# Kernel tuning notes

Hardware: AMD Instinct MI355X
Metric: run time of the kernel (lower is better)

The kernel has to match this reference:

```python
import jax, jax.numpy as jnp
import numpy as np

# ---- config (mirrors cfg in __init__) ----
XB = (-51.2, 51.2, 0.2)
YB = (-51.2, 51.2, 0.2)
ZB = (-10.0, 10.0, 20.0)
C_BEV = 64
BN_EPS = 1e-5

DX = jnp.array([XB[2], YB[2], ZB[2]], jnp.float32)
BX = jnp.array([XB[0] + XB[2] / 2, YB[0] + YB[2] / 2, ZB[0] + ZB[2] / 2], jnp.float32)
NX = (int((XB[1] - XB[0]) / XB[2]), int((YB[1] - YB[0]) / YB[2]), int((ZB[1] - ZB[0]) / ZB[2]))  # (512, 512, 1)


def setup_inputs() -> dict:
    key = jax.random.key(0)
    k1, k2, k3, k4 = jax.random.split(key, 4)
    B, N = 4, 100000
    xy = jax.random.uniform(k1, (B, N, 2), jnp.float32, -54.0, 54.0)   # some points out of bounds
    z = jax.random.uniform(k2, (B, N, 1), jnp.float32, -3.0, 3.0)
    inten = jax.random.uniform(k3, (B, N, 1), jnp.float32)
    points = jnp.concatenate([xy, z, inten], axis=-1)
    W = jax.random.normal(k4, (4, C_BEV), jnp.float32) * 0.5
    b = jnp.zeros((C_BEV,), jnp.float32)
    gamma = jnp.ones((C_BEV,), jnp.float32)
    beta = jnp.zeros((C_BEV,), jnp.float32)
    return {"points": points, "W": W, "b": b, "gamma": gamma, "beta": beta}


def reference(points, W, b, gamma, beta):
    B, N, _ = points.shape
    nx, ny, nz = NX
    p = points.reshape(-1, 4)                      # (B*N, 4)

    # PFN: Linear + BatchNorm1d (training-mode batch stats, biased var) + ReLU
    h = p @ W + b                                  # (B*N, C)
    mu = jnp.mean(h, axis=0)
    var = jnp.var(h, axis=0)
    feat = jax.nn.relu(gamma * (h - mu) * jax.lax.rsqrt(var + BN_EPS) + beta)

    # grid coords: torch .long() truncates toward zero; jnp astype(int) does too
    coords = ((p[:, :3] - (BX - DX / 2.0)) / DX).astype(jnp.int32)
    kept = ((coords[:, 0] >= 0) & (coords[:, 0] < nx)
            & (coords[:, 1] >= 0) & (coords[:, 1] < ny)
            & (coords[:, 2] >= 0) & (coords[:, 2] < nz))

    batch_ix = jnp.repeat(jnp.arange(B, dtype=jnp.int32), N)
    ranks = (batch_ix * (nx * ny * nz)
             + coords[:, 0] + coords[:, 1] * nx + coords[:, 2] * (nx * ny))

    # invalid points -> sentinel bucket (jit-safe replacement for boolean filtering).
    # segment_sum per unique rank == the sort + QuickCumsum trick + scatter-assign.
    flat = B * nx * ny * nz
    ranks = jnp.where(kept, ranks, flat)
    feat = jnp.where(kept[:, None], feat, 0.0)
    bev = jax.ops.segment_sum(feat, ranks, num_segments=flat + 1)[:flat]  # (flat, C)

    bev = bev.reshape(B, nz, ny, nx, C_BEV)
    bev = jnp.transpose(bev, (0, 4, 1, 2, 3)).sum(axis=2)  # (B, C, ny, nx)
    return bev
```

## Files before the change

kernel.cpp:

```cpp
#include <hip/hip_runtime.h>


#define NXG 512
#define NYXG (512 * 512)
#define CB 64
#define SBLK 256

__device__ __forceinline__ int coord_mul5(float x, float offx) {
    float t = x - offx;
    asm volatile("" : "+v"(t));
    float q = t * 5.0f;
    asm volatile("" : "+v"(q));
    return (int)q;
}

__global__ void zero_ints(int* __restrict__ p, int n) {
    int i = blockIdx.x * blockDim.x + threadIdx.x;
    if (i < n) p[i] = 0;
}

__global__ void zero_kernel(float4* __restrict__ p, long n4) {
    long i = (long)blockIdx.x * blockDim.x + threadIdx.x;
    long stride = (long)gridDim.x * blockDim.x;
    float4 z = make_float4(0.f, 0.f, 0.f, 0.f);
    for (; i < n4; i += stride) p[i] = z;
}

__global__ void stats_count(const float4* __restrict__ pts, const float* __restrict__ W,
                            double* __restrict__ S_part, int* __restrict__ counts,
                            int M, int Nper) {
    __shared__ float4 tile[256];
    __shared__ double sh1[256], sh2[256];
    int t = threadIdx.x;
    int lane = t & 63;
    int wv = t >> 6;
    float w0 = W[lane], w1 = W[64 + lane], w2 = W[128 + lane], w3 = W[192 + lane];
    const float offx = -51.1f - 0.1f;
    double s1 = 0.0, s2 = 0.0;

    int chunk = (M + gridDim.x - 1) / gridDim.x;
    int base = blockIdx.x * chunk;
    int end = base + chunk; if (end > M) end = M;

    for (int i0 = base; i0 < end; i0 += 256) {
        int n = end - i0; if (n > 256) n = 256;
        __syncthreads();
        if (t < n) {
            float4 p = pts[i0 + t];
            tile[t] = p;
            int cx = coord_mul5(p.x, offx);
            int cy = coord_mul5(p.y, offx);
            if (cx >= 0 && cx < NXG && cy >= 0 && cy < NXG) {
                int b = (i0 + t) / Nper;
                int bin = (((b << 9) + cy) << 2) | (cx >> 7);
                atomicAdd(&counts[bin], 1);
            }
        }
        __syncthreads();
        int j0 = wv * 64, j1 = j0 + 64; if (j1 > n) j1 = n;
        for (int j = j0; j < j1; ++j) {
            float4 p = tile[j];
            float q = p.x * w0 + p.y * w1 + p.z * w2 + p.w * w3;
            double qd = (double)q;
            s1 += qd;
            s2 += qd * qd;
        }
    }
    sh1[t] = s1;
    sh2[t] = s2;
    __syncthreads();
    if (t < 64) {
        int c = t;
        S_part[(long)blockIdx.x * 128 + c] =
            (sh1[c] + sh1[64 + c]) + (sh1[128 + c] + sh1[192 + c]);
        S_part[(long)blockIdx.x * 128 + 64 + c] =
            (sh2[c] + sh2[64 + c]) + (sh2[128 + c] + sh2[192 + c]);
    }
}

__global__ void reduce_finalize(const double* __restrict__ S_part,
                                const float* __restrict__ gamma, const float* __restrict__ beta,
                                float* __restrict__ AB, double invM) {
    __shared__ double sh[4][128];
    __shared__ double tot[128];
    int t = threadIdx.x;
    int g = t >> 7, tt = t & 127;
    const double* base = S_part + (long)g * 64 * 128 + tt;
    double a0 = 0.0, a1 = 0.0, a2 = 0.0, a3 = 0.0;
#pragma unroll
    for (int b = 0; b < 64; b += 4) {
        a0 += base[(long)(b + 0) * 128];
        a1 += base[(long)(b + 1) * 128];
        a2 += base[(long)(b + 2) * 128];
        a3 += base[(long)(b + 3) * 128];
    }
    sh[g][tt] = (a0 + a1) + (a2 + a3);
    __syncthreads();
    if (t < 128) tot[t] = (sh[0][t] + sh[1][t]) + (sh[2][t] + sh[3][t]);
    __syncthreads();
    if (t < 64) {
        double mu = tot[t] * invM;
        double var = tot[64 + t] * invM - mu * mu;
        double sc = (double)gamma[t] / sqrt(var + 1e-5);
        AB[t] = (float)sc;
        AB[64 + t] = (float)((double)beta[t] - mu * sc);
    }
}

__global__ void scan_kernel(const int* __restrict__ counts, int* __restrict__ start,
                            int* __restrict__ cursor, int NB) {
    __shared__ int partial[256];
    int t = threadIdx.x;
    int chunk = (NB + 255) >> 8;
    int i0 = t * chunk;
    int i1 = i0 + chunk; if (i1 > NB) i1 = NB; if (i0 > NB) i0 = NB;
    int s = 0;
    for (int i = i0; i < i1; ++i) s += counts[i];
    partial[t] = s;
    __syncthreads();
    if (t == 0) {
        int run = 0;
        for (int k = 0; k < 256; ++k) { int v = partial[k]; partial[k] = run; run += v; }
    }
    __syncthreads();
    int run = partial[t];
    for (int i = i0; i < i1; ++i) {
        int v = counts[i];
        start[i] = run;
        cursor[i] = run;
        run += v;
    }
    if (t == 255) start[NB] = run;
}

__global__ void reorder_kernel(const float4* __restrict__ pts, int* __restrict__ cursor,
                               float4* __restrict__ pts_s, int M, int Nper) {
    int i = blockIdx.x * blockDim.x + threadIdx.x;
    int stride = gridDim.x * blockDim.x;
    const float offx = -51.1f - 0.1f;
    for (; i < M; i += stride) {
        float4 p = pts[i];
        int cx = coord_mul5(p.x, offx);
        int cy = coord_mul5(p.y, offx);
        if (cx < 0 || cx >= NXG || cy < 0 || cy >= NXG) continue;
        int b = i / Nper;
        int bin = (((b << 9) + cy) << 2) | (cx >> 7);
        int idx = atomicAdd(&cursor[bin], 1);
        pts_s[idx] = p;
    }
}

__global__ __launch_bounds__(256) void gather_out(
    const float4* __restrict__ pts_s, const float* __restrict__ W,
    const float* __restrict__ AB, const int* __restrict__ bin_start,
    float* __restrict__ out) {
    __shared__ float acc[CB][129];
    __shared__ float4 ptile[64];
    int t = threadIdx.x;
    int lane = t & 63, wv = t >> 6;
    int bin = blockIdx.x;
    int quarter = bin & 3;
    int y = (bin >> 2) & 511;
    int b = bin >> 11;

    for (int k = t; k < CB * 129; k += 256) ((float*)acc)[k] = 0.f;

    float w0 = W[lane], w1 = W[64 + lane], w2 = W[128 + lane], w3 = W[192 + lane];
    float A = AB[lane], Bc = AB[64 + lane];
    const float offx = -51.1f - 0.1f;
    int s = bin_start[bin], e = bin_start[bin + 1];

    for (int i0 = s; i0 < e; i0 += 64) {
        int nn = e - i0; if (nn > 64) nn = 64;
        __syncthreads();
        if (t < nn) ptile[t] = pts_s[i0 + t];
        __syncthreads();
        for (int j = wv; j < nn; j += 4) {
            float4 p = ptile[j];
            int cx = coord_mul5(p.x, offx);
            int x = cx - (quarter << 7);
            float q = p.x * w0 + p.y * w1 + p.z * w2 + p.w * w3;
            float f = fmaxf(q * A + Bc, 0.f);
            atomicAdd(&acc[lane][x], f);
        }
    }
    __syncthreads();

    size_t obase = (size_t)b * CB * NYXG + (size_t)y * NXG + (quarter << 7);
#pragma unroll
    for (int j = 0; j < 8; ++j) {
        int idx = j * 256 + t;
        int c = idx >> 5;
        int xq = (idx & 31) << 2;
        float4 v = make_float4(acc[c][xq], acc[c][xq + 1],
                               acc[c][xq + 2], acc[c][xq + 3]);
        *(float4*)(out + obase + (size_t)c * NYXG + xq) = v;
    }
}

__global__ void scatter_direct(const float4* __restrict__ pts, const float* __restrict__ W,
                               const float* __restrict__ AB, float* __restrict__ out,
                               int M, int Nper) {
    int lane = threadIdx.x & 63;
    int wid = blockIdx.x * (blockDim.x >> 6) + (threadIdx.x >> 6);
    int nw = gridDim.x * (blockDim.x >> 6);
    float w0 = W[lane], w1 = W[64 + lane], w2 = W[128 + lane], w3 = W[192 + lane];
    float A = AB[lane], Bc = AB[64 + lane];
    const float offx = -51.1f - 0.1f;
    for (int i = wid; i < M; i += nw) {
        float4 p = pts[i];
        int cx = coord_mul5(p.x, offx);
        int cy = coord_mul5(p.y, offx);
        if (cx < 0 || cx >= NXG || cy < 0 || cy >= NXG) continue;
        int b = i / Nper;
        float q = p.x * w0 + p.y * w1 + p.z * w2 + p.w * w3;
        float f = fmaxf(q * A + Bc, 0.f);
        atomicAdd(&out[((long)(b * CB + lane) * NXG + cy) * NXG + cx], f);
    }
}

extern "C" void kernel_launch(void* const* d_in, const int* in_sizes, int n_in,
                              void* d_out, int out_size, void* d_ws, size_t ws_size,
                              hipStream_t stream) {
    const float4* pts = (const float4*)d_in[0];
    const float* W = (const float*)d_in[1];
    const float* gamma = (const float*)d_in[3];
    const float* beta = (const float*)d_in[4];
    float* out = (float*)d_out;

    int M = in_sizes[0] / 4;
    int B = out_size / (CB * NYXG);
    int Nper = M / B;
    int NB = B * 2048;

    char* wsb = (char*)d_ws;
    float* AB = (float*)(wsb + 1024);
    double* S_part = (double*)(wsb + 2048);

    size_t off = 2048 + (size_t)SBLK * 128 * sizeof(double);
    int* counts = (int*)(wsb + off);     off += (size_t)NB * 4;
    int* bin_start = (int*)(wsb + off);  off += (size_t)(NB + 1) * 4;
    int* bin_cursor = (int*)(wsb + off); off += (size_t)NB * 4;
    off = (off + 15) & ~(size_t)15;
    float4* pts_s = (float4*)(wsb + off); off += (size_t)M * 16;
    size_t need = off;

    if (ws_size >= need) {
        zero_ints<<<(NB + 255) / 256, 256, 0, stream>>>(counts, NB);
        stats_count<<<SBLK, 256, 0, stream>>>(pts, W, S_part, counts, M, Nper);
        reduce_finalize<<<1, 512, 0, stream>>>(S_part, gamma, beta, AB, 1.0 / (double)M);
        scan_kernel<<<1, 256, 0, stream>>>(counts, bin_start, bin_cursor, NB);
        reorder_kernel<<<1024, 256, 0, stream>>>(pts, bin_cursor, pts_s, M, Nper);
        gather_out<<<NB, 256, 0, stream>>>(pts_s, W, AB, bin_start, out);
    } else {
        zero_kernel<<<2048, 256, 0, stream>>>((float4*)out, (long)out_size / 4);
        stats_count<<<SBLK, 256, 0, stream>>>(pts, W, S_part, (int*)(wsb + 2048), M, Nper);
        reduce_finalize<<<1, 512, 0, stream>>>(S_part, gamma, beta, AB, 1.0 / (double)M);
        scatter_direct<<<2048, 256, 0, stream>>>(pts, W, AB, out, M, Nper);
    }
}
```

Measured before the change: 250.9 us.

## Restructure gather so each block owns one channel over a 16-row BEV strip

Points are now binned per (batch, row) instead of per (batch, row, x-quarter). The gather kernel assigns one block per (batch, 16-row strip, channel) and keeps a 16x512 shared accumulator, so each thread processes points independently with conflict-light shared atomics and writes one contiguous 32KB output region. The cost is that every point in a strip is re-read and re-projected once per channel, 64 times in total, in exchange for fully coalesced channel-plane stores and no per-point tile sync.

```diff
diff --git a/kernel.cpp b/kernel.cpp
--- a/kernel.cpp
+++ b/kernel.cpp
@@ -5,6 +5,7 @@
 #define NYXG (512 * 512)
 #define CB 64
 #define SBLK 256
+#define YCH 16
 
 __device__ __forceinline__ int coord_mul5(float x, float offx) {
     float t = x - offx;
@@ -52,8 +53,7 @@
             int cy = coord_mul5(p.y, offx);
             if (cx >= 0 && cx < NXG && cy >= 0 && cy < NXG) {
                 int b = (i0 + t) / Nper;
-                int bin = (((b << 9) + cy) << 2) | (cx >> 7);
-                atomicAdd(&counts[bin], 1);
+                atomicAdd(&counts[(b << 9) | cy], 1);
             }
         }
         __syncthreads();
@@ -144,8 +144,7 @@
         int cy = coord_mul5(p.y, offx);
         if (cx < 0 || cx >= NXG || cy < 0 || cy >= NXG) continue;
         int b = i / Nper;
-        int bin = (((b << 9) + cy) << 2) | (cx >> 7);
-        int idx = atomicAdd(&cursor[bin], 1);
+        int idx = atomicAdd(&cursor[(b << 9) | cy], 1);
         pts_s[idx] = p;
     }
 }
@@ -154,48 +153,37 @@
     const float4* __restrict__ pts_s, const float* __restrict__ W,
     const float* __restrict__ AB, const int* __restrict__ bin_start,
     float* __restrict__ out) {
-    __shared__ float acc[CB][129];
-    __shared__ float4 ptile[64];
-    int t = threadIdx.x;
-    int lane = t & 63, wv = t >> 6;
-    int bin = blockIdx.x;
-    int quarter = bin & 3;
-    int y = (bin >> 2) & 511;
-    int b = bin >> 11;
-
-    for (int k = t; k < CB * 129; k += 256) ((float*)acc)[k] = 0.f;
-
-    float w0 = W[lane], w1 = W[64 + lane], w2 = W[128 + lane], w3 = W[192 + lane];
-    float A = AB[lane], Bc = AB[64 + lane];
-    const float offx = -51.1f - 0.1f;
-    int s = bin_start[bin], e = bin_start[bin + 1];
-
-    for (int i0 = s; i0 < e; i0 += 64) {
-        int nn = e - i0; if (nn > 64) nn = 64;
-        __syncthreads();
-        if (t < nn) ptile[t] = pts_s[i0 + t];
-        __syncthreads();
-        for (int j = wv; j < nn; j += 4) {
-            float4 p = ptile[j];
-            int cx = coord_mul5(p.x, offx);
-            int x = cx - (quarter << 7);
-            float q = p.x * w0 + p.y * w1 + p.z * w2 + p.w * w3;
-            float f = fmaxf(q * A + Bc, 0.f);
-            atomicAdd(&acc[lane][x], f);
-        }
-    }
-    __syncthreads();
-
-    size_t obase = (size_t)b * CB * NYXG + (size_t)y * NXG + (quarter << 7);
+    __shared__ float acc[YCH][NXG];
+    int t = threadIdx.x;
+    int c = blockIdx.x & 63;
+    int yc = (blockIdx.x >> 6) & 31;
+    int b = blockIdx.x >> 11;
+
+    float4* az = (float4*)acc;
 #pragma unroll
-    for (int j = 0; j < 8; ++j) {
-        int idx = j * 256 + t;
-        int c = idx >> 5;
-        int xq = (idx & 31) << 2;
-        float4 v = make_float4(acc[c][xq], acc[c][xq + 1],
-                               acc[c][xq + 2], acc[c][xq + 3]);
-        *(float4*)(out + obase + (size_t)c * NYXG + xq) = v;
-    }
+    for (int j = t; j < YCH * NXG / 4; j += 256) az[j] = make_float4(0.f, 0.f, 0.f, 0.f);
+
+    float w0 = W[c], w1 = W[64 + c], w2 = W[128 + c], w3 = W[192 + c];
+    float A = AB[c], Bc = AB[64 + c];
+    const float offx = -51.1f - 0.1f;
+    int row0 = (b << 9) + (yc << 4);
+    int s = bin_start[row0], e = bin_start[row0 + YCH];
+    __syncthreads();
+
+    for (int i = s + t; i < e; i += 256) {
+        float4 p = pts_s[i];
+        int cx = coord_mul5(p.x, offx);
+        int cy = coord_mul5(p.y, offx);
+        int row = cy - (yc << 4);
+        float q = p.x * w0 + p.y * w1 + p.z * w2 + p.w * w3;
+        float f = fmaxf(q * A + Bc, 0.f);
+        atomicAdd(&acc[row][cx], f);
+    }
+    __syncthreads();
+
+    float4* o4 = (float4*)(out + ((size_t)(b * CB + c) * NXG + (yc << 4)) * NXG);
+#pragma unroll
+    for (int j = t; j < YCH * NXG / 4; j += 256) o4[j] = az[j];
 }
 
 __global__ void scatter_direct(const float4* __restrict__ pts, const float* __restrict__ W,
@@ -231,7 +219,7 @@
     int M = in_sizes[0] / 4;
     int B = out_size / (CB * NYXG);
     int Nper = M / B;
-    int NB = B * 2048;
+    int NB = B * 512;
 
     char* wsb = (char*)d_ws;
     float* AB = (float*)(wsb + 1024);
@@ -251,7 +239,7 @@
         reduce_finalize<<<1, 512, 0, stream>>>(S_part, gamma, beta, AB, 1.0 / (double)M);
         scan_kernel<<<1, 256, 0, stream>>>(counts, bin_start, bin_cursor, NB);
         reorder_kernel<<<1024, 256, 0, stream>>>(pts, bin_cursor, pts_s, M, Nper);
-        gather_out<<<NB, 256, 0, stream>>>(pts_s, W, AB, bin_start, out);
+        gather_out<<<B * 32 * 64, 256, 0, stream>>>(pts_s, W, AB, bin_start, out);
     } else {
         zero_kernel<<<2048, 256, 0, stream>>>((float4*)out, (long)out_size / 4);
         stats_count<<<SBLK, 256, 0, stream>>>(pts, W, S_part, (int*)(wsb + 2048), M, Nper);
```

Measured after the change: 252.2 us. No clear change (+0.5%).
